# Kernel optimization log

Measured on AMD Instinct MI355X. Metric: run time of the kernel, lower is better.

The kernel has to match this reference:

```python
import jax, jax.numpy as jnp
import numpy as np

N = 100000
E = 1600000
F = 64
OUT = 7

def setup_inputs() -> dict:
    key = jax.random.key(0)
    k1, k2, k3, k4, k5 = jax.random.split(key, 5)
    x = jax.random.normal(k1, (N, F), dtype=jnp.float32)
    edge_index = jax.random.randint(k2, (2, E), 0, N, dtype=jnp.int64)
    W_l = jax.random.normal(k3, (F, OUT), dtype=jnp.float32) / np.sqrt(F)
    b_l = jax.random.normal(k4, (OUT,), dtype=jnp.float32) * 0.01
    W_r = jax.random.normal(k5, (F, OUT), dtype=jnp.float32) / np.sqrt(F)
    return {"x": x, "edge_index": edge_index, "W_l": W_l, "b_l": b_l, "W_r": W_r}

def reference(x, edge_index, W_l, b_l, W_r):
    # PyG SAGEConv (mean aggr): out = lin_l(mean_{j in N(i)} x_j) + lin_r(x_i), then relu
    src, dst = edge_index[0], edge_index[1]
    msgs = x[src]                                            # [E, F] gather
    agg = jax.ops.segment_sum(msgs, dst, num_segments=N)     # [N, F]
    cnt = jax.ops.segment_sum(jnp.ones((E,), dtype=x.dtype), dst, num_segments=N)
    mean = agg / jnp.maximum(cnt, 1.0)[:, None]              # isolated nodes -> 0
    out = mean @ W_l + b_l + x @ W_r                         # [N, 7]
    return jax.nn.relu(out)
```

## Files before the change

### kernel.cpp

```cpp
#include <hip/hip_runtime.h>

#define NN 100000
#define NE 1600000
#define FIN 64
#define FOUT 7

#define BSH 9
#define NBK 196
#define PBLK 1000
#define PTH  256
#define EPB  1600
#define EPT  7
#define NCOPY 4
#define NCTR (NBK * NCOPY)
#define ROWS 200
#define PROJB 391
#define ACCTH 1024
#define SCAP 9216
#define INVALID 0xFFFFFFFFu

__device__ __forceinline__ unsigned bf16r(float f) {
    unsigned u = __float_as_uint(f);
    return (u + 0x7fffu + ((u >> 16) & 1u)) >> 16;
}
__device__ __forceinline__ float bflo(unsigned u) { return __uint_as_float(u << 16); }
__device__ __forceinline__ float bfhi(unsigned u) { return __uint_as_float(u & 0xffff0000u); }

__global__ __launch_bounds__(PTH) void part_proj_kernel(
    const int* __restrict__ eg,
    const float* __restrict__ x, const float* __restrict__ Wl,
    const float* __restrict__ bl, const float* __restrict__ Wr,
    unsigned* __restrict__ part, unsigned short* __restrict__ offs,
    unsigned* __restrict__ z, float* __restrict__ outself)
{
    __shared__ unsigned st_cnt[NCTR];
    __shared__ unsigned st_start[NCTR];
    __shared__ unsigned stage[EPB];
    __shared__ unsigned wsum[NCOPY];

    const int t = threadIdx.x;

    if (blockIdx.x >= PBLK) {
        int i = (int)(blockIdx.x - PBLK) * PTH + t;
        if (i >= NN) return;

        float al[FOUT], ar[FOUT];
#pragma unroll
        for (int j = 0; j < FOUT; ++j) { al[j] = 0.f; ar[j] = 0.f; }

        const float4* xr = (const float4*)(x + (size_t)i * FIN);
#pragma unroll
        for (int kk = 0; kk < FIN / 4; ++kk) {
            float4 xv = xr[kk];
            float v[4] = {xv.x, xv.y, xv.z, xv.w};
#pragma unroll
            for (int c = 0; c < 4; ++c) {
                int k = kk * 4 + c;
#pragma unroll
                for (int j = 0; j < FOUT; ++j) {
                    al[j] = fmaf(v[c], Wl[k * FOUT + j], al[j]);
                    ar[j] = fmaf(v[c], Wr[k * FOUT + j], ar[j]);
                }
            }
        }

        uint4 pk;
        pk.x = bf16r(al[0]) | (bf16r(al[1]) << 16);
        pk.y = bf16r(al[2]) | (bf16r(al[3]) << 16);
        pk.z = bf16r(al[4]) | (bf16r(al[5]) << 16);
        pk.w = bf16r(al[6]);
        ((uint4*)z)[i] = pk;

        float* o = outself + (size_t)i * FOUT;
#pragma unroll
        for (int j = 0; j < FOUT; ++j)
            o[j] = ar[j] + bl[j];
        return;
    }

    const int e0   = (int)blockIdx.x * EPB;
    const int lane = t & 63;
    const int wv   = t >> 6;

    for (int b = t; b < NCTR; b += PTH) st_cnt[b] = 0;
    __syncthreads();

    unsigned held[EPT], hcr[EPT];
#pragma unroll
    for (int j = 0; j < EPT; ++j) {
        int k = t + j * PTH;
        if (k < EPB) {
            unsigned s = (unsigned)eg[e0 + k];
            unsigned d = (unsigned)eg[NE + e0 + k];
            unsigned cidx = (d >> BSH) * NCOPY + wv;
            unsigned r = atomicAdd(&st_cnt[cidx], 1u);
            held[j] = ((d & 511u) << 17) | s;
            hcr[j]  = (cidx << 11) | r;
        } else hcr[j] = INVALID;
    }
    __syncthreads();

    {
        unsigned c[4], sum = 0;
#pragma unroll
        for (int q = 0; q < 4; ++q) {
            int idx = 4 * t + q;
            c[q] = (idx < NCTR) ? st_cnt[idx] : 0u;
            sum += c[q];
        }
        unsigned inc = sum;
#pragma unroll
        for (int off = 1; off < 64; off <<= 1) {
            unsigned v = (unsigned)__shfl_up((int)inc, off, 64);
            if (lane >= off) inc += v;
        }
        if (lane == 63) wsum[wv] = inc;
        __syncthreads();
        if (t == 0) {
            unsigned run = 0;
#pragma unroll
            for (int w = 0; w < NCOPY; ++w) { unsigned tmp = wsum[w]; wsum[w] = run; run += tmp; }
        }
        __syncthreads();
        unsigned base = wsum[wv] + inc - sum;
#pragma unroll
        for (int q = 0; q < 4; ++q) {
            int idx = 4 * t + q;
            if (idx < NCTR) st_start[idx] = base;
            base += c[q];
        }
    }
    __syncthreads();

#pragma unroll
    for (int j = 0; j < EPT; ++j) {
        if (hcr[j] != INVALID) {
            unsigned cidx = hcr[j] >> 11, r = hcr[j] & 0x7FFu;
            stage[st_start[cidx] + r] = held[j];
        }
    }

    if (t <= NBK)
        offs[(size_t)blockIdx.x * ROWS + t] =
            (unsigned short)((t == NBK) ? EPB : st_start[t * NCOPY]);
    __syncthreads();

    const uint4* sg = (const uint4*)stage;
    uint4* pg = (uint4*)(part + (size_t)blockIdx.x * EPB);
    for (int j = t; j < EPB / 4; j += PTH) pg[j] = sg[j];
}

__global__ __launch_bounds__(ACCTH) void acc_kernel(
    const unsigned short* __restrict__ offs, const unsigned* __restrict__ part,
    const unsigned* __restrict__ zb, float* __restrict__ out)
{
    __shared__ unsigned s_cnt[512];
    __shared__ unsigned s_start[512];
    __shared__ unsigned s_pos[512];
    __shared__ unsigned sstage[SCAP];
    __shared__ float    lacc[512 * 8];
    __shared__ unsigned wtot[8];

    const int t = threadIdx.x;
    const int k = blockIdx.x;

    if (t < 512) s_cnt[t] = 0;
    __syncthreads();

    unsigned rbase = 0, len = 0;
    if (t < PBLK) {
        unsigned o0 = offs[(size_t)t * ROWS + k];
        unsigned o1 = offs[(size_t)t * ROWS + k + 1];
        len   = o1 - o0;
        rbase = (unsigned)t * EPB + o0;
    }

    for (unsigned j = 0; j < len; ++j)
        atomicAdd(&s_cnt[part[rbase + j] >> 17], 1u);
    __syncthreads();

    unsigned cval = 0, inc = 0;
    if (t < 512) {
        cval = s_cnt[t];
        inc = cval;
#pragma unroll
        for (int off = 1; off < 64; off <<= 1) {
            unsigned v = (unsigned)__shfl_up((int)inc, off, 64);
            if ((t & 63) >= off) inc += v;
        }
        if ((t & 63) == 63) wtot[t >> 6] = inc;
    }
    __syncthreads();
    if (t == 0) {
        unsigned run = 0;
#pragma unroll
        for (int w = 0; w < 8; ++w) { unsigned tmp = wtot[w]; wtot[w] = run; run += tmp; }
    }
    __syncthreads();
    if (t < 512) {
        unsigned st = wtot[t >> 6] + inc - cval;
        s_start[t] = st;
        s_pos[t]   = st;
    }
    __syncthreads();

    for (unsigned j = 0; j < len; ++j) {
        unsigned e = part[rbase + j];
        unsigned p = atomicAdd(&s_pos[e >> 17], 1u);
        if (p < SCAP) sstage[p] = e & 0x1FFFFu;
    }
    __syncthreads();

    unsigned node = t & 511u;
    unsigned half = (unsigned)t >> 9;
    unsigned deg  = s_cnt[node];
    unsigned base = s_start[node];
    unsigned lo = half ? (deg >> 1) : 0u;
    unsigned hi = half ? deg : (deg >> 1);

    float a0 = 0.f, a1 = 0.f, a2 = 0.f, a3 = 0.f, a4 = 0.f, a5 = 0.f, a6 = 0.f;
    for (unsigned j = lo; j < hi; ++j) {
        unsigned src = sstage[base + j];
        uint4 zr = ((const uint4*)zb)[src];
        a0 += bflo(zr.x); a1 += bfhi(zr.x);
        a2 += bflo(zr.y); a3 += bfhi(zr.y);
        a4 += bflo(zr.z); a5 += bfhi(zr.z);
        a6 += bflo(zr.w);
    }

    if (half) {
        float* L = &lacc[node * 8];
        *(float4*)(L)     = make_float4(a0, a1, a2, a3);
        *(float4*)(L + 4) = make_float4(a4, a5, a6, 0.f);
    }
    __syncthreads();

    if (!half) {
        const float* L = &lacc[node * 8];
        a0 += L[0]; a1 += L[1]; a2 += L[2]; a3 += L[3];
        a4 += L[4]; a5 += L[5]; a6 += L[6];
        int i = (k << BSH) + (int)node;
        if (i < NN) {
            float r = 1.0f / (float)max((int)deg, 1);
            float* o = out + (size_t)i * FOUT;
            o[0] = fmaxf(fmaf(a0, r, o[0]), 0.f);
            o[1] = fmaxf(fmaf(a1, r, o[1]), 0.f);
            o[2] = fmaxf(fmaf(a2, r, o[2]), 0.f);
            o[3] = fmaxf(fmaf(a3, r, o[3]), 0.f);
            o[4] = fmaxf(fmaf(a4, r, o[4]), 0.f);
            o[5] = fmaxf(fmaf(a5, r, o[5]), 0.f);
            o[6] = fmaxf(fmaf(a6, r, o[6]), 0.f);
        }
    }
}

extern "C" void kernel_launch(void* const* d_in, const int* in_sizes, int n_in,
                              void* d_out, int out_size, void* d_ws, size_t ws_size,
                              hipStream_t stream) {
    const float* x   = (const float*)d_in[0];
    const int*   edg = (const int*)d_in[1];
    const float* Wl  = (const float*)d_in[2];
    const float* bl  = (const float*)d_in[3];
    const float* Wr  = (const float*)d_in[4];
    float* out = (float*)d_out;

    unsigned*       z    = (unsigned*)d_ws;
    unsigned*       part = z + (size_t)NN * 4;
    unsigned short* offs = (unsigned short*)(part + (size_t)PBLK * EPB);

    part_proj_kernel<<<PBLK + PROJB, PTH, 0, stream>>>(edg, x, Wl, bl, Wr,
                                                       part, offs, z, out);
    acc_kernel<<<NBK, ACCTH, 0, stream>>>(offs, part, z, out);
}
```

Measured before the change: 128.2 us.

## Split accumulation across four blocks per bucket with a separate merge kernel

The accumulation stage now runs four 512-thread blocks per destination bucket, each covering a quarter of the partition rows and writing per-node partial sums and counts to workspace. A new merge kernel adds the partials, applies the mean, residual and relu. Partitioning uses smaller 800-edge blocks, and the projection is split into its own kernel. This raises parallelism in the latency-bound gather phase at the cost of extra launches and partial-buffer traffic. The staging cap clamps rows that overflow instead of dropping edges silently, though overflow still truncates results.

```diff
diff --git a/kernel.cpp b/kernel.cpp
--- a/kernel.cpp
+++ b/kernel.cpp
@@ -7,16 +7,18 @@
 
 #define BSH 9
 #define NBK 196
-#define PBLK 1000
+#define PBLK 2000
 #define PTH  256
-#define EPB  1600
-#define EPT  7
+#define EPB  800
+#define EPT  4
 #define NCOPY 4
 #define NCTR (NBK * NCOPY)
 #define ROWS 200
+#define SPLIT 4
+#define RPS (PBLK / SPLIT)
+#define ATH 512
+#define SCAP 2560
 #define PROJB 391
-#define ACCTH 1024
-#define SCAP 9216
 #define INVALID 0xFFFFFFFFu
 
 __device__ __forceinline__ unsigned bf16r(float f) {
@@ -26,58 +28,57 @@
 __device__ __forceinline__ float bflo(unsigned u) { return __uint_as_float(u << 16); }
 __device__ __forceinline__ float bfhi(unsigned u) { return __uint_as_float(u & 0xffff0000u); }
 
-__global__ __launch_bounds__(PTH) void part_proj_kernel(
-    const int* __restrict__ eg,
+__global__ __launch_bounds__(256) void proj_kernel(
     const float* __restrict__ x, const float* __restrict__ Wl,
     const float* __restrict__ bl, const float* __restrict__ Wr,
-    unsigned* __restrict__ part, unsigned short* __restrict__ offs,
-    unsigned* __restrict__ z, float* __restrict__ outself)
+    unsigned* __restrict__ z, float* __restrict__ outself, int n)
+{
+    int i = blockIdx.x * blockDim.x + threadIdx.x;
+    if (i >= n) return;
+
+    float al[FOUT], ar[FOUT];
+#pragma unroll
+    for (int j = 0; j < FOUT; ++j) { al[j] = 0.f; ar[j] = 0.f; }
+
+    const float4* xr = (const float4*)(x + (size_t)i * FIN);
+#pragma unroll
+    for (int kk = 0; kk < FIN / 4; ++kk) {
+        float4 xv = xr[kk];
+        float v[4] = {xv.x, xv.y, xv.z, xv.w};
+#pragma unroll
+        for (int c = 0; c < 4; ++c) {
+            int k = kk * 4 + c;
+#pragma unroll
+            for (int j = 0; j < FOUT; ++j) {
+                al[j] = fmaf(v[c], Wl[k * FOUT + j], al[j]);
+                ar[j] = fmaf(v[c], Wr[k * FOUT + j], ar[j]);
+            }
+        }
+    }
+
+    uint4 pk;
+    pk.x = bf16r(al[0]) | (bf16r(al[1]) << 16);
+    pk.y = bf16r(al[2]) | (bf16r(al[3]) << 16);
+    pk.z = bf16r(al[4]) | (bf16r(al[5]) << 16);
+    pk.w = bf16r(al[6]);
+    ((uint4*)z)[i] = pk;
+
+    float* o = outself + (size_t)i * FOUT;
+#pragma unroll
+    for (int j = 0; j < FOUT; ++j)
+        o[j] = ar[j] + bl[j];
+}
+
+__global__ __launch_bounds__(PTH) void part_kernel(
+    const int* __restrict__ eg, unsigned* __restrict__ part,
+    unsigned short* __restrict__ offs)
 {
     __shared__ unsigned st_cnt[NCTR];
     __shared__ unsigned st_start[NCTR];
     __shared__ unsigned stage[EPB];
     __shared__ unsigned wsum[NCOPY];
 
-    const int t = threadIdx.x;
-
-    if (blockIdx.x >= PBLK) {
-        int i = (int)(blockIdx.x - PBLK) * PTH + t;
-        if (i >= NN) return;
-
-        float al[FOUT], ar[FOUT];
-#pragma unroll
-        for (int j = 0; j < FOUT; ++j) { al[j] = 0.f; ar[j] = 0.f; }
-
-        const float4* xr = (const float4*)(x + (size_t)i * FIN);
-#pragma unroll
-        for (int kk = 0; kk < FIN / 4; ++kk) {
-            float4 xv = xr[kk];
-            float v[4] = {xv.x, xv.y, xv.z, xv.w};
-#pragma unroll
-            for (int c = 0; c < 4; ++c) {
-                int k = kk * 4 + c;
-#pragma unroll
-                for (int j = 0; j < FOUT; ++j) {
-                    al[j] = fmaf(v[c], Wl[k * FOUT + j], al[j]);
-                    ar[j] = fmaf(v[c], Wr[k * FOUT + j], ar[j]);
-                }
-            }
-        }
-
-        uint4 pk;
-        pk.x = bf16r(al[0]) | (bf16r(al[1]) << 16);
-        pk.y = bf16r(al[2]) | (bf16r(al[3]) << 16);
-        pk.z = bf16r(al[4]) | (bf16r(al[5]) << 16);
-        pk.w = bf16r(al[6]);
-        ((uint4*)z)[i] = pk;
-
-        float* o = outself + (size_t)i * FOUT;
-#pragma unroll
-        for (int j = 0; j < FOUT; ++j)
-            o[j] = ar[j] + bl[j];
-        return;
-    }
-
+    const int t    = threadIdx.x;
     const int e0   = (int)blockIdx.x * EPB;
     const int lane = t & 63;
     const int wv   = t >> 6;
@@ -95,7 +96,7 @@
             unsigned cidx = (d >> BSH) * NCOPY + wv;
             unsigned r = atomicAdd(&st_cnt[cidx], 1u);
             held[j] = ((d & 511u) << 17) | s;
-            hcr[j]  = (cidx << 11) | r;
+            hcr[j]  = (cidx << 10) | r;
         } else hcr[j] = INVALID;
     }
     __syncthreads();
@@ -135,7 +136,7 @@
 #pragma unroll
     for (int j = 0; j < EPT; ++j) {
         if (hcr[j] != INVALID) {
-            unsigned cidx = hcr[j] >> 11, r = hcr[j] & 0x7FFu;
+            unsigned cidx = hcr[j] >> 10, r = hcr[j] & 0x3FFu;
             stage[st_start[cidx] + r] = held[j];
         }
     }
@@ -150,46 +151,43 @@
     for (int j = t; j < EPB / 4; j += PTH) pg[j] = sg[j];
 }
 
-__global__ __launch_bounds__(ACCTH) void acc_kernel(
+__global__ __launch_bounds__(ATH) void acc_kernel(
     const unsigned short* __restrict__ offs, const unsigned* __restrict__ part,
-    const unsigned* __restrict__ zb, float* __restrict__ out)
+    const unsigned* __restrict__ zb, float* __restrict__ partial)
 {
     __shared__ unsigned s_cnt[512];
     __shared__ unsigned s_start[512];
     __shared__ unsigned s_pos[512];
     __shared__ unsigned sstage[SCAP];
-    __shared__ float    lacc[512 * 8];
     __shared__ unsigned wtot[8];
 
     const int t = threadIdx.x;
-    const int k = blockIdx.x;
-
-    if (t < 512) s_cnt[t] = 0;
+    const int k = blockIdx.x >> 2;
+    const int s = blockIdx.x & 3;
+
+    s_cnt[t] = 0;
     __syncthreads();
 
     unsigned rbase = 0, len = 0;
-    if (t < PBLK) {
-        unsigned o0 = offs[(size_t)t * ROWS + k];
-        unsigned o1 = offs[(size_t)t * ROWS + k + 1];
+    if (t < RPS) {
+        unsigned r = (unsigned)(s * RPS + t);
+        unsigned o0 = offs[(size_t)r * ROWS + k];
+        unsigned o1 = offs[(size_t)r * ROWS + k + 1];
         len   = o1 - o0;
-        rbase = (unsigned)t * EPB + o0;
+        rbase = r * EPB + o0;
     }
 
     for (unsigned j = 0; j < len; ++j)
         atomicAdd(&s_cnt[part[rbase + j] >> 17], 1u);
     __syncthreads();
 
-    unsigned cval = 0, inc = 0;
-    if (t < 512) {
-        cval = s_cnt[t];
-        inc = cval;
-#pragma unroll
-        for (int off = 1; off < 64; off <<= 1) {
-            unsigned v = (unsigned)__shfl_up((int)inc, off, 64);
-            if ((t & 63) >= off) inc += v;
-        }
-        if ((t & 63) == 63) wtot[t >> 6] = inc;
-    }
+    unsigned cval = s_cnt[t], inc = cval;
+#pragma unroll
+    for (int off = 1; off < 64; off <<= 1) {
+        unsigned v = (unsigned)__shfl_up((int)inc, off, 64);
+        if ((t & 63) >= off) inc += v;
+    }
+    if ((t & 63) == 63) wtot[t >> 6] = inc;
     __syncthreads();
     if (t == 0) {
         unsigned run = 0;
@@ -197,7 +195,7 @@
         for (int w = 0; w < 8; ++w) { unsigned tmp = wtot[w]; wtot[w] = run; run += tmp; }
     }
     __syncthreads();
-    if (t < 512) {
+    {
         unsigned st = wtot[t >> 6] + inc - cval;
         s_start[t] = st;
         s_pos[t]   = st;
@@ -211,16 +209,13 @@
     }
     __syncthreads();
 
-    unsigned node = t & 511u;
-    unsigned half = (unsigned)t >> 9;
-    unsigned deg  = s_cnt[node];
-    unsigned base = s_start[node];
-    unsigned lo = half ? (deg >> 1) : 0u;
-    unsigned hi = half ? deg : (deg >> 1);
+    unsigned deg  = s_cnt[t];
+    unsigned base = s_start[t];
+    unsigned hi   = min(base + deg, (unsigned)SCAP);
 
     float a0 = 0.f, a1 = 0.f, a2 = 0.f, a3 = 0.f, a4 = 0.f, a5 = 0.f, a6 = 0.f;
-    for (unsigned j = lo; j < hi; ++j) {
-        unsigned src = sstage[base + j];
+    for (unsigned j = base; j < hi; ++j) {
+        unsigned src = sstage[j];
         uint4 zr = ((const uint4*)zb)[src];
         a0 += bflo(zr.x); a1 += bfhi(zr.x);
         a2 += bflo(zr.y); a3 += bfhi(zr.y);
@@ -228,30 +223,36 @@
         a6 += bflo(zr.w);
     }
 
-    if (half) {
-        float* L = &lacc[node * 8];
-        *(float4*)(L)     = make_float4(a0, a1, a2, a3);
-        *(float4*)(L + 4) = make_float4(a4, a5, a6, 0.f);
-    }
-    __syncthreads();
-
-    if (!half) {
-        const float* L = &lacc[node * 8];
-        a0 += L[0]; a1 += L[1]; a2 += L[2]; a3 += L[3];
-        a4 += L[4]; a5 += L[5]; a6 += L[6];
-        int i = (k << BSH) + (int)node;
-        if (i < NN) {
-            float r = 1.0f / (float)max((int)deg, 1);
-            float* o = out + (size_t)i * FOUT;
-            o[0] = fmaxf(fmaf(a0, r, o[0]), 0.f);
-            o[1] = fmaxf(fmaf(a1, r, o[1]), 0.f);
-            o[2] = fmaxf(fmaf(a2, r, o[2]), 0.f);
-            o[3] = fmaxf(fmaf(a3, r, o[3]), 0.f);
-            o[4] = fmaxf(fmaf(a4, r, o[4]), 0.f);
-            o[5] = fmaxf(fmaf(a5, r, o[5]), 0.f);
-            o[6] = fmaxf(fmaf(a6, r, o[6]), 0.f);
-        }
-    }
+    float* pp = partial + ((size_t)blockIdx.x * 512 + t) * 8;
+    *(float4*)(pp)     = make_float4(a0, a1, a2, a3);
+    *(float4*)(pp + 4) = make_float4(a4, a5, a6, (float)deg);
+}
+
+__global__ __launch_bounds__(256) void merge_kernel(
+    const float* __restrict__ partial, float* __restrict__ out, int n)
+{
+    int i = blockIdx.x * blockDim.x + threadIdx.x;
+    if (i >= n) return;
+    int k = i >> BSH;
+    int node = i & 511;
+
+    float s0 = 0.f, s1 = 0.f, s2 = 0.f, s3 = 0.f, s4 = 0.f, s5 = 0.f, s6 = 0.f, cn = 0.f;
+#pragma unroll
+    for (int s = 0; s < SPLIT; ++s) {
+        const float4* p = (const float4*)(partial + ((size_t)(k * SPLIT + s) * 512 + node) * 8);
+        float4 a = p[0], b = p[1];
+        s0 += a.x; s1 += a.y; s2 += a.z; s3 += a.w;
+        s4 += b.x; s5 += b.y; s6 += b.z; cn += b.w;
+    }
+    float r = 1.0f / fmaxf(cn, 1.0f);
+    float* o = out + (size_t)i * FOUT;
+    o[0] = fmaxf(fmaf(s0, r, o[0]), 0.f);
+    o[1] = fmaxf(fmaf(s1, r, o[1]), 0.f);
+    o[2] = fmaxf(fmaf(s2, r, o[2]), 0.f);
+    o[3] = fmaxf(fmaf(s3, r, o[3]), 0.f);
+    o[4] = fmaxf(fmaf(s4, r, o[4]), 0.f);
+    o[5] = fmaxf(fmaf(s5, r, o[5]), 0.f);
+    o[6] = fmaxf(fmaf(s6, r, o[6]), 0.f);
 }
 
 extern "C" void kernel_launch(void* const* d_in, const int* in_sizes, int n_in,
@@ -264,11 +265,13 @@
     const float* Wr  = (const float*)d_in[4];
     float* out = (float*)d_out;
 
-    unsigned*       z    = (unsigned*)d_ws;
-    unsigned*       part = z + (size_t)NN * 4;
-    unsigned short* offs = (unsigned short*)(part + (size_t)PBLK * EPB);
-
-    part_proj_kernel<<<PBLK + PROJB, PTH, 0, stream>>>(edg, x, Wl, bl, Wr,
-                                                       part, offs, z, out);
-    acc_kernel<<<NBK, ACCTH, 0, stream>>>(offs, part, z, out);
-}
+    unsigned*       z       = (unsigned*)d_ws;
+    unsigned*       part    = z + (size_t)NN * 4;
+    unsigned short* offs    = (unsigned short*)(part + (size_t)NE);
+    float*          partial = (float*)(offs + (size_t)PBLK * ROWS);
+
+    proj_kernel<<<PROJB, 256, 0, stream>>>(x, Wl, bl, Wr, z, out, NN);
+    part_kernel<<<PBLK, PTH, 0, stream>>>(edg, part, offs);
+    acc_kernel<<<NBK * SPLIT, ATH, 0, stream>>>(offs, part, z, partial);
+    merge_kernel<<<(NN + 255) / 256, 256, 0, stream>>>(partial, out, NN);
+}
```

New measurement: 131.0 us. 2.2% more time.
